# Kernel tuning notes

Hardware: AMD Instinct MI355X
Metric: run time of the kernel (lower is better)

The kernel has to match this reference:

```python
import jax, jax.numpy as jnp
import numpy as np

D_MODEL = 1024
N_HEADS = 16
D_K = D_MODEL // N_HEADS
LN_EPS = 1e-5


def setup_inputs() -> dict:
    key = jax.random.key(0)
    ks = jax.random.split(key, 11)
    s = 1.0 / np.sqrt(D_MODEL)
    x = jax.random.normal(ks[0], (4, 2048, D_MODEL), dtype=jnp.float32)
    W_q = jax.random.uniform(ks[1], (D_MODEL, D_MODEL), jnp.float32, -s, s)
    b_q = jax.random.uniform(ks[2], (D_MODEL,), jnp.float32, -s, s)
    W_k = jax.random.uniform(ks[3], (D_MODEL, D_MODEL), jnp.float32, -s, s)
    b_k = jax.random.uniform(ks[4], (D_MODEL,), jnp.float32, -s, s)
    W_v = jax.random.uniform(ks[5], (D_MODEL, D_MODEL), jnp.float32, -s, s)
    b_v = jax.random.uniform(ks[6], (D_MODEL,), jnp.float32, -s, s)
    W_o = jax.random.uniform(ks[7], (D_MODEL, D_MODEL), jnp.float32, -s, s)
    b_o = jax.random.uniform(ks[8], (D_MODEL,), jnp.float32, -s, s)
    ln_gamma = jnp.ones((D_MODEL,), jnp.float32)
    ln_beta = jnp.zeros((D_MODEL,), jnp.float32)
    return {"x": x, "W_q": W_q, "b_q": b_q, "W_k": W_k, "b_k": b_k,
            "W_v": W_v, "b_v": b_v, "W_o": W_o, "b_o": b_o,
            "ln_gamma": ln_gamma, "ln_beta": ln_beta}


def reference(x, W_q, b_q, W_k, b_k, W_v, b_v, W_o, b_o, ln_gamma, ln_beta):
    B, S, D = x.shape
    # Linear projections (torch Linear: x @ W.T + b); split into heads.
    def proj(W, b):
        y = jnp.einsum('bsd,ed->bse', x, W) + b
        return y.reshape(B, S, N_HEADS, D_K).transpose(0, 2, 1, 3)  # [B,H,S,dk]
    Q = proj(W_q, b_q)
    K = proj(W_k, b_k)
    V = proj(W_v, b_v)
    scores = jnp.einsum('bhqd,bhkd->bhqk', Q, K) / np.sqrt(D_K)
    attn = jax.nn.softmax(scores, axis=-1)  # dropout is identity in eval
    context = jnp.einsum('bhqk,bhkd->bhqd', attn, V)
    context = context.transpose(0, 2, 1, 3).reshape(B, S, D)
    out = jnp.einsum('bsd,ed->bse', context, W_o) + b_o
    h = x + out  # residual
    mu = jnp.mean(h, axis=-1, keepdims=True)
    var = jnp.mean(jnp.square(h - mu), axis=-1, keepdims=True)
    return (h - mu) / jnp.sqrt(var + LN_EPS) * ln_gamma + ln_beta
```

## Files before the change

### kernel.cpp

```cpp
#include <hip/hip_runtime.h>
#include <hip/hip_bf16.h>
#include <stdint.h>

typedef __attribute__((ext_vector_type(4))) float f32x4;
typedef __attribute__((ext_vector_type(8))) short bf16x8;
typedef __attribute__((ext_vector_type(4))) short bf16x4;
typedef __attribute__((ext_vector_type(4))) short s16x4;

__device__ __forceinline__ float b2f(short s) {
    union { uint32_t u; float f; } v; v.u = ((uint32_t)(uint16_t)s) << 16; return v.f;
}
__device__ __forceinline__ short f2b(float f) {
    union { float f; uint32_t u; } v; v.f = f;
    uint32_t r = v.u + 0x7FFF + ((v.u >> 16) & 1);
    return (short)(r >> 16);
}
__device__ __forceinline__ f32x4 zero4() { f32x4 z = {0.f, 0.f, 0.f, 0.f}; return z; }

__device__ __forceinline__ void async16(const void* g, void* l) {
    __builtin_amdgcn_global_load_lds(
        (const __attribute__((address_space(1))) void*)g,
        (__attribute__((address_space(3))) void*)l, 16, 0, 0);
}
__device__ __forceinline__ uint32_t lds_addr(const void* p) {
    return (uint32_t)(uintptr_t)(const __attribute__((address_space(3))) void*)p;
}
__device__ __forceinline__ float exp2fast(float x) {
    float r; asm("v_exp_f32 %0, %1" : "=v"(r) : "v"(x)); return r;
}
__device__ __forceinline__ uint32_t cvtpk(float lo, float hi) {
    uint32_t r; asm("v_cvt_pk_bf16_f32 %0, %1, %2" : "=v"(r) : "v"(lo), "v"(hi)); return r;
}

__global__ __launch_bounds__(256)
void cvt5(const float* __restrict__ x,
          const float* __restrict__ wq, const float* __restrict__ wk,
          const float* __restrict__ wv, const float* __restrict__ wo,
          short* __restrict__ xb, short* __restrict__ wqb, short* __restrict__ wkb,
          short* __restrict__ wvb, short* __restrict__ wob)
{
    const int b = blockIdx.x;
    const float* src; short* dst; size_t off;
    if (b < 8192) { src = x; dst = xb; off = (size_t)b * 1024; }
    else {
        const int wsel = (b - 8192) >> 10;
        off = (size_t)((b - 8192) & 1023) * 1024;
        switch (wsel) {
            case 0: src = wq; dst = wqb; break;
            case 1: src = wk; dst = wkb; break;
            case 2: src = wv; dst = wvb; break;
            default: src = wo; dst = wob; break;
        }
    }
    const int t = threadIdx.x;
    const float4 v = *(const float4*)(src + off + t * 4);
    s16x4 o;
    o[0] = f2b(v.x); o[1] = f2b(v.y); o[2] = f2b(v.z); o[3] = f2b(v.w);
    *(s16x4*)(dst + off + t * 4) = o;
}

template <bool OUTF32, bool RESID>
__device__ __forceinline__
void gemm_core(const short* __restrict__ Ab, const short* __restrict__ Bb,
               const float* __restrict__ bias, const float* __restrict__ resid,
               void* __restrict__ Cv, int m0, int n0col, int K, int N,
               short* lsA, short* lsB)
{
    const int t = threadIdx.x;
    const int wave = t >> 6, lane = t & 63;
    const int wr = wave >> 1, wc = wave & 1;
    const int lr = lane & 15, kg = lane >> 4;

    f32x4 acc[4][4];
#pragma unroll
    for (int m = 0; m < 4; ++m)
#pragma unroll
        for (int n = 0; n < 4; ++n) acc[m][n] = zero4();

    const int rG = t >> 3;
    const int cG = (((t & 7) ^ (rG & 7))) * 8;

    for (int k0 = 0; k0 < K; k0 += 64) {
        __syncthreads();
#pragma unroll
        for (int i = 0; i < 4; ++i) {
            async16(Ab + (size_t)(rG + 32 * i) * K + k0 + cG, &lsA[t * 8 + 2048 * i]);
            async16(Bb + (size_t)(rG + 32 * i) * K + k0 + cG, &lsB[t * 8 + 2048 * i]);
        }
        __syncthreads();

#pragma unroll
        for (int ks = 0; ks < 2; ++ks) {
            const int xc = ((ks * 4 + kg) ^ (lr & 7)) * 8;
            bf16x8 aF[4], bF[4];
#pragma unroll
            for (int m = 0; m < 4; ++m)
                aF[m] = *(const bf16x8*)&lsA[(wr * 64 + m * 16 + lr) * 64 + xc];
#pragma unroll
            for (int n = 0; n < 4; ++n)
                bF[n] = *(const bf16x8*)&lsB[(wc * 64 + n * 16 + lr) * 64 + xc];
#pragma unroll
            for (int m = 0; m < 4; ++m)
#pragma unroll
                for (int n = 0; n < 4; ++n)
                    acc[m][n] = __builtin_amdgcn_mfma_f32_16x16x32_bf16(aF[m], bF[n], acc[m][n], 0, 0, 0);
        }
    }

#pragma unroll
    for (int n = 0; n < 4; ++n) {
        const int col = n0col + wc * 64 + n * 16 + lr;
        const float bvv = bias[col - n0col + n0col];
#pragma unroll
        for (int m = 0; m < 4; ++m) {
            const int rowb = m0 + wr * 64 + m * 16 + kg * 4;
#pragma unroll
            for (int r = 0; r < 4; ++r) {
                const size_t idx = (size_t)(rowb + r) * N + col;
                float v = acc[m][n][r] + bvv;
                if (RESID) v += resid[idx];
                if (OUTF32) ((float*)Cv)[idx] = v;
                else        ((short*)Cv)[idx] = f2b(v);
            }
        }
    }
}

__global__ __launch_bounds__(256)
void gemm_qkv(const short* __restrict__ A, const short* __restrict__ Wcat,
              const float* __restrict__ bq, const float* __restrict__ bk,
              const float* __restrict__ bv,
              short* __restrict__ Qw, short* __restrict__ Kw, short* __restrict__ Vw)
{
    __shared__ short lsA[128 * 64];
    __shared__ short lsB[128 * 64];
    const int nb = blockIdx.x;
    const int tb = nb >> 3;
    const float* bias = (tb == 0) ? bq : (tb == 1) ? bk : bv;
    short* dst = (tb == 0) ? Qw : (tb == 1) ? Kw : Vw;
    gemm_core<false, false>(A + (size_t)blockIdx.y * 128 * 1024,
                            Wcat + (size_t)nb * 128 * 1024,
                            bias - (nb & 7) * 128,
                            nullptr, dst, blockIdx.y * 128, (nb & 7) * 128, 1024, 1024,
                            lsA, lsB);
}

__global__ __launch_bounds__(256)
void gemm_out(const short* __restrict__ A, const short* __restrict__ Bw,
              const float* __restrict__ bias, const float* __restrict__ resid,
              float* __restrict__ C)
{
    __shared__ short lsA[128 * 64];
    __shared__ short lsB[128 * 64];
    gemm_core<true, true>(A + (size_t)blockIdx.y * 128 * 1024,
                          Bw + (size_t)blockIdx.x * 128 * 1024,
                          bias, resid, C, blockIdx.y * 128, blockIdx.x * 128, 1024, 1024,
                          lsA, lsB);
}

__global__ __launch_bounds__(256)
void attn_fwd(const short* __restrict__ Q, const short* __restrict__ K,
              const short* __restrict__ V, short* __restrict__ ctx)
{
    __shared__ short lsK[2][64 * 64];
    __shared__ short lsV[2][64 * 64];
    __shared__ short lsP[4][16 * 64];

    const float C1 = 0.18033688011112042f;

    const int t = threadIdx.x, w = t >> 6, lane = t & 63;
    const int lr = lane & 15, kg = lane >> 4;
    const int bh = blockIdx.x;
    const size_t base = (size_t)(bh >> 4) * 2048 * 1024 + (size_t)(bh & 15) * 64;
    const short* Qg = Q + base;
    const short* Kg = K + base;
    const short* Vg = V + base;
    short* Og = ctx + base;
    const int q0 = blockIdx.y * 128 + w * 32;

    bf16x8 qB[2][2];
#pragma unroll
    for (int m = 0; m < 2; ++m)
#pragma unroll
        for (int ks = 0; ks < 2; ++ks)
            qB[m][ks] = *(const bf16x8*)(Qg + (size_t)(q0 + m * 16 + lr) * 1024 + ks * 32 + kg * 8);

    const int rK  = t >> 3;
    const int cK  = (((t & 7) ^ (rK & 7))) * 8;
    const int kvV = (t & 127) >> 1;
    const int dV0 = ((t >> 7) << 4) + (t & 1) * 8;
    const int dV1 = dV0 + 32;

    f32x4 o[2][4];
#pragma unroll
    for (int m = 0; m < 2; ++m)
#pragma unroll
        for (int n = 0; n < 4; ++n) o[m][n] = zero4();
    float mx[2] = {-1e30f, -1e30f};
    float lsum[2] = {0.f, 0.f};

    const int pmask = (lr & 7) << 3;
    short* lsPw = lsP[w];

    async16(Kg + (size_t)rK * 1024 + cK,        &lsK[0][t * 8]);
    async16(Kg + (size_t)(32 + rK) * 1024 + cK, &lsK[0][t * 8 + 2048]);
    async16(Vg + (size_t)kvV * 1024 + dV0,      &lsV[0][t * 8]);
    async16(Vg + (size_t)kvV * 1024 + dV1,      &lsV[0][t * 8 + 2048]);

    int buf = 0;
    for (int it = 0; it < 32; ++it) {
        __syncthreads();
        if (it + 1 < 32) {
            const int kv0 = (it + 1) * 64;
            short* bK = lsK[buf ^ 1]; short* bV = lsV[buf ^ 1];
            async16(Kg + (size_t)(kv0 + rK) * 1024 + cK,      bK + t * 8);
            async16(Kg + (size_t)(kv0 + 32 + rK) * 1024 + cK, bK + t * 8 + 2048);
            async16(Vg + (size_t)(kv0 + kvV) * 1024 + dV0,    bV + t * 8);
            async16(Vg + (size_t)(kv0 + kvV) * 1024 + dV1,    bV + t * 8 + 2048);
        }
        const short* cbK = lsK[buf];
        const short* cbV = lsV[buf];

        f32x4 s[2][4];
        const int x0 = ((kg)     ^ (lr & 7)) * 8;
        const int x1 = ((4 + kg) ^ (lr & 7)) * 8;
        __builtin_amdgcn_s_setprio(1);
#pragma unroll
        for (int cb = 0; cb < 4; ++cb) {
            const bf16x8 kA0 = *(const bf16x8*)&cbK[(cb * 16 + lr) * 64 + x0];
            const bf16x8 kA1 = *(const bf16x8*)&cbK[(cb * 16 + lr) * 64 + x1];
#pragma unroll
            for (int m = 0; m < 2; ++m) {
                f32x4 a = __builtin_amdgcn_mfma_f32_16x16x32_bf16(kA0, qB[m][0], zero4(), 0, 0, 0);
                s[m][cb] = __builtin_amdgcn_mfma_f32_16x16x32_bf16(kA1, qB[m][1], a, 0, 0, 0);
            }
        }
        __builtin_amdgcn_s_setprio(0);

        float smax[2];
#pragma unroll
        for (int m = 0; m < 2; ++m) {
            float a = fmaxf(fmaxf(s[m][0][0], s[m][0][1]), fmaxf(s[m][0][2], s[m][0][3]));
            float b = fmaxf(fmaxf(s[m][1][0], s[m][1][1]), fmaxf(s[m][1][2], s[m][1][3]));
            float c = fmaxf(fmaxf(s[m][2][0], s[m][2][1]), fmaxf(s[m][2][2], s[m][2][3]));
            float d = fmaxf(fmaxf(s[m][3][0], s[m][3][1]), fmaxf(s[m][3][2], s[m][3][3]));
            float e = fmaxf(fmaxf(a, b), fmaxf(c, d));
            e = fmaxf(e, __shfl_xor(e, 16));
            e = fmaxf(e, __shfl_xor(e, 32));
            smax[m] = e;
        }

        if (!__all((smax[0] <= mx[0] + 64.f) && (smax[1] <= mx[1] + 64.f))) {
            float corrS[2];
#pragma unroll
            for (int m = 0; m < 2; ++m) {
                const float mnew = fmaxf(mx[m], smax[m]);
                corrS[m] = exp2fast((mx[m] - mnew) * C1);
                mx[m] = mnew;
                lsum[m] *= corrS[m];
            }
#pragma unroll
            for (int m = 0; m < 2; ++m) {
                f32x4 c;
#pragma unroll
                for (int r = 0; r < 4; ++r) c[r] = __shfl(corrS[m], kg * 4 + r);
#pragma unroll
                for (int n = 0; n < 4; ++n) {
                    o[m][n][0] *= c[0]; o[m][n][1] *= c[1];
                    o[m][n][2] *= c[2]; o[m][n][3] *= c[3];
                }
            }
        }

        bf16x4 tv[4][4];
#pragma unroll
        for (int n = 0; n < 4; ++n) {
            const uint32_t a = lds_addr(&cbV[n * 1024 + kg * 128 + lr]);
            asm volatile(
                "ds_read_b64_tr_b16 %0, %4\n\t"
                "ds_read_b64_tr_b16 %1, %4 offset:128\n\t"
                "ds_read_b64_tr_b16 %2, %4 offset:1024\n\t"
                "ds_read_b64_tr_b16 %3, %4 offset:1152"
                : "=&v"(tv[n][0]), "=&v"(tv[n][1]), "=&v"(tv[n][2]), "=&v"(tv[n][3])
                : "v"(a));
        }
        asm volatile("s_waitcnt lgkmcnt(0)" ::: "memory");
        __builtin_amdgcn_sched_barrier(0);

#pragma unroll
        for (int m = 0; m < 2; ++m) {
            const float nm2 = mx[m] * C1;
            float tsum = 0.f;
#pragma unroll
            for (int cb = 0; cb < 4; ++cb) {
                const float p0 = exp2fast(fmaf(s[m][cb][0], C1, -nm2));
                const float p1 = exp2fast(fmaf(s[m][cb][1], C1, -nm2));
                const float p2 = exp2fast(fmaf(s[m][cb][2], C1, -nm2));
                const float p3 = exp2fast(fmaf(s[m][cb][3], C1, -nm2));
                tsum += (p0 + p1) + (p2 + p3);
                const int c0i = (cb * 16 + kg * 4) ^ pmask;
                *(uint32_t*)&lsPw[lr * 64 + c0i]     = cvtpk(p0, p1);
                *(uint32_t*)&lsPw[lr * 64 + c0i + 2] = cvtpk(p2, p3);
            }
            tsum += __shfl_xor(tsum, 16);
            tsum += __shfl_xor(tsum, 32);
            lsum[m] += tsum;

            bf16x8 pA[2];
#pragma unroll
            for (int kh = 0; kh < 2; ++kh)
                pA[kh] = *(const bf16x8*)&lsPw[lr * 64 + ((kh * 32 + kg * 8) ^ pmask)];

            __builtin_amdgcn_s_setprio(1);
#pragma unroll
            for (int n = 0; n < 4; ++n) {
#pragma unroll
                for (int kh = 0; kh < 2; ++kh) {
                    const bf16x8 vB = __builtin_shufflevector(tv[n][kh * 2], tv[n][kh * 2 + 1],
                                                              0, 1, 2, 3, 4, 5, 6, 7);
                    o[m][n] = __builtin_amdgcn_mfma_f32_16x16x32_bf16(pA[kh], vB, o[m][n], 0, 0, 0);
                }
            }
            __builtin_amdgcn_s_setprio(0);
        }
        buf ^= 1;
    }

#pragma unroll
    for (int m = 0; m < 2; ++m) {
        f32x4 inv;
#pragma unroll
        for (int r = 0; r < 4; ++r) inv[r] = 1.0f / __shfl(lsum[m], kg * 4 + r);
#pragma unroll
        for (int n = 0; n < 4; ++n)
#pragma unroll
            for (int r = 0; r < 4; ++r) {
                const int row = q0 + m * 16 + kg * 4 + r;
                Og[(size_t)row * 1024 + n * 16 + lr] = f2b(o[m][n][r] * inv[r]);
            }
    }
}

__global__ __launch_bounds__(256)
void ln_inplace(float* __restrict__ io, const float* __restrict__ gamma,
                const float* __restrict__ beta)
{
    __shared__ float redS[4];
    __shared__ float redQ[4];
    const int t = threadIdx.x, wave = t >> 6, lane = t & 63;
    const size_t rb = (size_t)blockIdx.x * 1024;

    float4 v4 = *(const float4*)&io[rb + t * 4];
    float v[4] = {v4.x, v4.y, v4.z, v4.w};

    float s = 0.f, sq = 0.f;
#pragma unroll
    for (int j = 0; j < 4; ++j) { s += v[j]; sq += v[j] * v[j]; }
#pragma unroll
    for (int off = 32; off; off >>= 1) {
        s  += __shfl_xor(s, off);
        sq += __shfl_xor(sq, off);
    }
    if (lane == 0) { redS[wave] = s; redQ[wave] = sq; }
    __syncthreads();
    const float mean = (redS[0] + redS[1] + redS[2] + redS[3]) * (1.0f / 1024.0f);
    const float ex2  = (redQ[0] + redQ[1] + redQ[2] + redQ[3]) * (1.0f / 1024.0f);
    const float var  = fmaxf(ex2 - mean * mean, 0.f);
    const float inv  = rsqrtf(var + 1e-5f);

    float4 o4;
    o4.x = (v[0] - mean) * inv * gamma[t * 4 + 0] + beta[t * 4 + 0];
    o4.y = (v[1] - mean) * inv * gamma[t * 4 + 1] + beta[t * 4 + 1];
    o4.z = (v[2] - mean) * inv * gamma[t * 4 + 2] + beta[t * 4 + 2];
    o4.w = (v[3] - mean) * inv * gamma[t * 4 + 3] + beta[t * 4 + 3];
    *(float4*)&io[rb + t * 4] = o4;
}

extern "C" void kernel_launch(void* const* d_in, const int* in_sizes, int n_in,
                              void* d_out, int out_size, void* d_ws, size_t ws_size,
                              hipStream_t stream)
{
    const float* x  = (const float*)d_in[0];
    const float* Wq = (const float*)d_in[1];
    const float* bq = (const float*)d_in[2];
    const float* Wk = (const float*)d_in[3];
    const float* bk = (const float*)d_in[4];
    const float* Wv = (const float*)d_in[5];
    const float* bv = (const float*)d_in[6];
    const float* Wo = (const float*)d_in[7];
    const float* bo = (const float*)d_in[8];
    const float* gamma = (const float*)d_in[9];
    const float* beta  = (const float*)d_in[10];

    const size_t NX = (size_t)8192 * 1024;
    const size_t NW = (size_t)1024 * 1024;

    short* xb  = (short*)d_ws;
    short* Wqb = xb + NX;
    short* Wkb = Wqb + NW;
    short* Wvb = Wkb + NW;
    short* Wob = Wvb + NW;
    short* Qw  = Wob + NW;
    short* Kw  = Qw + NX;
    short* Vw  = Kw + NX;
    short* Cw  = Vw + NX;
    float* out = (float*)d_out;

    dim3 blk(256);
    cvt5<<<dim3(12288), blk, 0, stream>>>(x, Wq, Wk, Wv, Wo, xb, Wqb, Wkb, Wvb, Wob);
    gemm_qkv<<<dim3(24, 64), blk, 0, stream>>>(xb, Wqb, bq, bk, bv, Qw, Kw, Vw);
    attn_fwd<<<dim3(64, 16), blk, 0, stream>>>(Qw, Kw, Vw, Cw);
    gemm_out<<<dim3(8, 64), blk, 0, stream>>>(Cw, Wob, bo, x, out);
    ln_inplace<<<dim3(8192), blk, 0, stream>>>(out, gamma, beta);
}
```

Baseline: 240.9 us.

## Double attention block to 8 waves sharing K/V tiles, defer row-sum reduction

The attention kernel now runs 512 threads (8 waves) per block covering 256 queries, so each K/V tile loaded into LDS is shared by twice as many waves. Each thread issues one async load per tile instead of two, using incrementing pointers. The per-iteration cross-lane reduction of the softmax row sum moves to the epilogue, which removes shuffles from the inner loop. The trade-off is a larger LDS footprint and fewer, bigger blocks, which can lower occupancy and give a coarser load balance across the grid.

```diff
diff --git a/kernel.cpp b/kernel.cpp
--- a/kernel.cpp
+++ b/kernel.cpp
@@ -110,7 +110,7 @@
 #pragma unroll
     for (int n = 0; n < 4; ++n) {
         const int col = n0col + wc * 64 + n * 16 + lr;
-        const float bvv = bias[col - n0col + n0col];
+        const float bvv = bias[col];
 #pragma unroll
         for (int m = 0; m < 4; ++m) {
             const int rowb = m0 + wr * 64 + m * 16 + kg * 4;
@@ -158,13 +158,13 @@
                           lsA, lsB);
 }
 
-__global__ __launch_bounds__(256)
+__global__ __launch_bounds__(512)
 void attn_fwd(const short* __restrict__ Q, const short* __restrict__ K,
               const short* __restrict__ V, short* __restrict__ ctx)
 {
     __shared__ short lsK[2][64 * 64];
     __shared__ short lsV[2][64 * 64];
-    __shared__ short lsP[4][16 * 64];
+    __shared__ short lsP[8][16 * 64];
 
     const float C1 = 0.18033688011112042f;
 
@@ -173,10 +173,8 @@
     const int bh = blockIdx.x;
     const size_t base = (size_t)(bh >> 4) * 2048 * 1024 + (size_t)(bh & 15) * 64;
     const short* Qg = Q + base;
-    const short* Kg = K + base;
-    const short* Vg = V + base;
     short* Og = ctx + base;
-    const int q0 = blockIdx.y * 128 + w * 32;
+    const int q0 = blockIdx.y * 256 + w * 32;
 
     bf16x8 qB[2][2];
 #pragma unroll
@@ -188,8 +186,9 @@
     const int rK  = t >> 3;
     const int cK  = (((t & 7) ^ (rK & 7))) * 8;
     const int kvV = (t & 127) >> 1;
-    const int dV0 = ((t >> 7) << 4) + (t & 1) * 8;
-    const int dV1 = dV0 + 32;
+    const int dV  = ((t >> 7) << 4) + (t & 1) * 8;
+    const short* pK = K + base + (size_t)rK * 1024 + cK;
+    const short* pV = V + base + (size_t)kvV * 1024 + dV;
 
     f32x4 o[2][4];
 #pragma unroll
@@ -202,21 +201,16 @@
     const int pmask = (lr & 7) << 3;
     short* lsPw = lsP[w];
 
-    async16(Kg + (size_t)rK * 1024 + cK,        &lsK[0][t * 8]);
-    async16(Kg + (size_t)(32 + rK) * 1024 + cK, &lsK[0][t * 8 + 2048]);
-    async16(Vg + (size_t)kvV * 1024 + dV0,      &lsV[0][t * 8]);
-    async16(Vg + (size_t)kvV * 1024 + dV1,      &lsV[0][t * 8 + 2048]);
+    async16(pK, &lsK[0][t * 8]);
+    async16(pV, &lsV[0][t * 8]);
 
     int buf = 0;
     for (int it = 0; it < 32; ++it) {
         __syncthreads();
         if (it + 1 < 32) {
-            const int kv0 = (it + 1) * 64;
-            short* bK = lsK[buf ^ 1]; short* bV = lsV[buf ^ 1];
-            async16(Kg + (size_t)(kv0 + rK) * 1024 + cK,      bK + t * 8);
-            async16(Kg + (size_t)(kv0 + 32 + rK) * 1024 + cK, bK + t * 8 + 2048);
-            async16(Vg + (size_t)(kv0 + kvV) * 1024 + dV0,    bV + t * 8);
-            async16(Vg + (size_t)(kv0 + kvV) * 1024 + dV1,    bV + t * 8 + 2048);
+            pK += 65536; pV += 65536;
+            async16(pK, &lsK[buf ^ 1][t * 8]);
+            async16(pV, &lsV[buf ^ 1][t * 8]);
         }
         const short* cbK = lsK[buf];
         const short* cbV = lsV[buf];
@@ -302,8 +296,6 @@
                 *(uint32_t*)&lsPw[lr * 64 + c0i]     = cvtpk(p0, p1);
                 *(uint32_t*)&lsPw[lr * 64 + c0i + 2] = cvtpk(p2, p3);
             }
-            tsum += __shfl_xor(tsum, 16);
-            tsum += __shfl_xor(tsum, 32);
             lsum[m] += tsum;
 
             bf16x8 pA[2];
@@ -328,9 +320,12 @@
 
 #pragma unroll
     for (int m = 0; m < 2; ++m) {
+        float lp = lsum[m];
+        lp += __shfl_xor(lp, 16);
+        lp += __shfl_xor(lp, 32);
         f32x4 inv;
 #pragma unroll
-        for (int r = 0; r < 4; ++r) inv[r] = 1.0f / __shfl(lsum[m], kg * 4 + r);
+        for (int r = 0; r < 4; ++r) inv[r] = 1.0f / __shfl(lp, kg * 4 + r);
 #pragma unroll
         for (int n = 0; n < 4; ++n)
 #pragma unroll
@@ -406,10 +401,9 @@
     short* Cw  = Vw + NX;
     float* out = (float*)d_out;
 
-    dim3 blk(256);
-    cvt5<<<dim3(12288), blk, 0, stream>>>(x, Wq, Wk, Wv, Wo, xb, Wqb, Wkb, Wvb, Wob);
-    gemm_qkv<<<dim3(24, 64), blk, 0, stream>>>(xb, Wqb, bq, bk, bv, Qw, Kw, Vw);
-    attn_fwd<<<dim3(64, 16), blk, 0, stream>>>(Qw, Kw, Vw, Cw);
-    gemm_out<<<dim3(8, 64), blk, 0, stream>>>(Cw, Wob, bo, x, out);
-    ln_inplace<<<dim3(8192), blk, 0, stream>>>(out, gamma, beta);
-}
+    cvt5<<<dim3(12288), dim3(256), 0, stream>>>(x, Wq, Wk, Wv, Wo, xb, Wqb, Wkb, Wvb, Wob);
+    gemm_qkv<<<dim3(24, 64), dim3(256), 0, stream>>>(xb, Wqb, bq, bk, bv, Qw, Kw, Vw);
+    attn_fwd<<<dim3(64, 8), dim3(512), 0, stream>>>(Qw, Kw, Vw, Cw);
+    gemm_out<<<dim3(8, 64), dim3(256), 0, stream>>>(Cw, Wob, bo, x, out);
+    ln_inplace<<<dim3(8192), dim3(256), 0, stream>>>(out, gamma, beta);
+}
```

After: 243.5 us. Within noise of the previous version (+1.1%).
